# Kernel tuning notes

Hardware: AMD Instinct MI355X
Metric: run time of the kernel (lower is better)

## Reference

```python
import jax, jax.numpy as jnp
import numpy as np
from jax import lax

B, T, H = 4096, 2048, 32


def setup_inputs() -> dict:
    key = jax.random.key(0)
    ks = jax.random.split(key, 10)
    s = 1.0 / np.sqrt(H)  # PyTorch LSTM/Linear init scale
    x = jax.random.normal(ks[0], (B, T, 1), dtype=jnp.float32)
    lengths = jax.random.randint(ks[1], (B,), 1, T + 1, dtype=jnp.int32)
    u = lambda k, shape, sc: jax.random.uniform(k, shape, jnp.float32, -sc, sc)
    return {
        "x": x,
        "lengths": lengths,
        # backward-direction LSTM weights (only h_n[-1] is used by the head)
        "w_ih": u(ks[2], (4 * H, 1), s),
        "w_hh": u(ks[3], (4 * H, H), s),
        "b_ih": u(ks[4], (4 * H,), s),
        "b_hh": u(ks[5], (4 * H,), s),
        "fc_w": u(ks[6], (64, H), 1.0 / np.sqrt(H)),
        "fc_b": u(ks[7], (64,), 1.0 / np.sqrt(H)),
        "fc2_w": u(ks[8], (1, 64), 1.0 / np.sqrt(64)),
        "fc2_b": u(ks[9], (1,), 1.0 / np.sqrt(64)),
    }


def _backward_lstm_final(x, lengths, w_ih, w_hh, b_ih, b_hh):
    """Final hidden state of the backward direction of a packed BiLSTM.

    The backward direction reads each sequence from t=len-1 down to t=0 with
    zero initial state. Equivalently: scan padded x in reverse time order and
    only update (h, c) where t < length (packed-sequence semantics).
    """
    Bv, Tv, _ = x.shape
    ts = jnp.arange(Tv - 1, -1, -1)                       # reversed time indices
    xs_t = jnp.transpose(x[:, ::-1, :], (1, 0, 2))        # [T, B, 1]
    mask_t = ts[:, None] < lengths[None, :]               # [T, B]

    def step(carry, inp):
        h, c = carry
        xt, m = inp                                        # [B,1], [B]
        gates = xt @ w_ih.T + b_ih + h @ w_hh.T + b_hh     # [B, 4H]
        i, f, g, o = jnp.split(gates, 4, axis=-1)
        i = jax.nn.sigmoid(i)
        f = jax.nn.sigmoid(f)
        g = jnp.tanh(g)
        o = jax.nn.sigmoid(o)
        c_new = f * c + i * g
        h_new = o * jnp.tanh(c_new)
        mm = m[:, None]
        return (jnp.where(mm, h_new, h), jnp.where(mm, c_new, c)), None

    h0 = jnp.zeros((Bv, H), dtype=x.dtype)
    c0 = jnp.zeros((Bv, H), dtype=x.dtype)
    (h_n, _), _ = lax.scan(step, (h0, c0), (xs_t, mask_t))
    return h_n                                             # [B, H]


def reference(x, lengths, w_ih, w_hh, b_ih, b_hh, fc_w, fc_b, fc2_w, fc2_b):
    h_n = _backward_lstm_final(x, lengths, w_ih, w_hh, b_ih, b_hh)
    out = jax.nn.elu(h_n @ fc_w.T + fc_b)                  # [B, 64]
    out = jax.nn.sigmoid(out @ fc2_w.T + fc2_b)            # [B, 1]
    return out
```

## Files before the change

### kernel.cpp

```cpp
#include <hip/hip_runtime.h>
#include <hip/hip_bf16.h>

constexpr int BB = 4096;
constexpr int TT = 2048;
constexpr int HH = 32;

typedef float v2f __attribute__((ext_vector_type(2)));
typedef float v4f __attribute__((ext_vector_type(4)));
typedef _Float16 v2h __attribute__((ext_vector_type(2)));
typedef _Float16 v8h __attribute__((ext_vector_type(8)));

__device__ __forceinline__ float fexp2(float x) { return __builtin_amdgcn_exp2f(x); }
__device__ __forceinline__ float frcp(float x)  { return __builtin_amdgcn_rcpf(x); }
__device__ __forceinline__ float fsigmoid(float x) {
    return frcp(1.0f + fexp2(x * -1.4426950408889634f));
}
__device__ __forceinline__ float felu(float x) {
    return x > 0.0f ? x : (fexp2(x * 1.4426950408889634f) - 1.0f);
}

__global__ void sort_by_len_kernel(const int* __restrict__ lengths, int* __restrict__ perm) {
    __shared__ int hist[TT];
    __shared__ int csum[256];
    const int tid = threadIdx.x;
    for (int i = tid; i < TT; i += 256) hist[i] = 0;
    __syncthreads();
    for (int i = tid; i < BB; i += 256) atomicAdd(&hist[TT - lengths[i]], 1);
    __syncthreads();
    const int base = tid * 8;
    int loc[8];
    int s = 0;
#pragma unroll
    for (int j = 0; j < 8; ++j) { loc[j] = hist[base + j]; s += loc[j]; }
    csum[tid] = s;
    __syncthreads();
    for (int off = 1; off < 256; off <<= 1) {
        int v = (tid >= off) ? csum[tid - off] : 0;
        __syncthreads();
        csum[tid] += v;
        __syncthreads();
    }
    int run = csum[tid] - s;
#pragma unroll
    for (int j = 0; j < 8; ++j) { int t = loc[j]; hist[base + j] = run; run += t; }
    __syncthreads();
    for (int i = tid; i < BB; i += 256) {
        int pos = atomicAdd(&hist[TT - lengths[i]], 1);
        perm[pos] = i;
    }
}

__global__ __attribute__((amdgpu_flat_work_group_size(64, 64), amdgpu_waves_per_eu(1, 4)))
void lstm_kernel(const float* __restrict__ x, const int* __restrict__ lengths,
                 const float* __restrict__ w_ih, const float* __restrict__ w_hh,
                 const float* __restrict__ b_ih, const float* __restrict__ b_hh,
                 const float* __restrict__ fc_w, const float* __restrict__ fc_b,
                 const float* __restrict__ fc2_w, const float* __restrict__ fc2_b,
                 float* __restrict__ out, const int* __restrict__ perm) {
    __shared__ __align__(16) _Float16 hs[64];
    __shared__ float xbuf[64];

    const int lane = threadIdx.x;
    const int b = perm ? perm[blockIdx.x] : blockIdx.x;
    const int L = lengths[b];

    const int r0 = lane;
    const int r1 = lane + 64;

    const bool  lower  = lane < 32;
    const float NL2E   = -1.4426950408889634f;
    const float scale0 = NL2E;
    const float scale1 = lower ? 2.0f * NL2E : NL2E;
    const float amul   = lower ? 2.0f : 1.0f;
    const float badd   = lower ? -1.0f : 0.0f;

    v2h w0[16], w1[16];
    {
        const v2f* p0 = reinterpret_cast<const v2f*>(w_hh + r0 * 32);
        const v2f* p1 = reinterpret_cast<const v2f*>(w_hh + r1 * 32);
#pragma unroll
        for (int q = 0; q < 16; ++q) {
            v2f a = p0[q]; v2f bq = p1[q];
            w0[q] = (v2h){(_Float16)(a.x * scale0), (_Float16)(a.y * scale0)};
            w1[q] = (v2h){(_Float16)(bq.x * scale1), (_Float16)(bq.y * scale1)};
        }
    }
    float wi0 = w_ih[r0] * scale0;
    float wi1 = w_ih[r1] * scale1;
    float bi0 = (b_ih[r0] + b_hh[r0]) * scale0;
    float bi1 = (b_ih[r1] + b_hh[r1]) * scale1;

#pragma unroll
    for (int q = 0; q < 16; ++q) {
        asm volatile("" : "+v"(w0[q]), "+v"(w1[q]));
    }

    v8h hr[4];
#pragma unroll
    for (int q = 0; q < 4; ++q) hr[q] = (v8h)(_Float16)0.0f;
    float c = 0.0f;
    const float* xb = x + (size_t)b * TT;

    int t = L - 1;
    while (t >= 0) {
        const int tb = t & ~63;
        xbuf[lane] = xb[tb + lane];
        for (; t >= tb; --t) {
            const float xt = xbuf[t - tb];
            float a0  = fmaf(wi0, xt, bi0);
            float a1  = fmaf(wi1, xt, bi1);
            float a0b = 0.0f, a1b = 0.0f;
#pragma unroll
            for (int q = 0; q < 4; ++q) {
                const v8h hh = hr[q];
                const v2h p01 = __builtin_shufflevector(hh, hh, 0, 1);
                const v2h p23 = __builtin_shufflevector(hh, hh, 2, 3);
                const v2h p45 = __builtin_shufflevector(hh, hh, 4, 5);
                const v2h p67 = __builtin_shufflevector(hh, hh, 6, 7);
                a0  = __builtin_amdgcn_fdot2(w0[4*q+0], p01, a0,  false);
                a0b = __builtin_amdgcn_fdot2(w0[4*q+1], p23, a0b, false);
                a0  = __builtin_amdgcn_fdot2(w0[4*q+2], p45, a0,  false);
                a0b = __builtin_amdgcn_fdot2(w0[4*q+3], p67, a0b, false);
                a1  = __builtin_amdgcn_fdot2(w1[4*q+0], p01, a1,  false);
                a1b = __builtin_amdgcn_fdot2(w1[4*q+1], p23, a1b, false);
                a1  = __builtin_amdgcn_fdot2(w1[4*q+2], p45, a1,  false);
                a1b = __builtin_amdgcn_fdot2(w1[4*q+3], p67, a1b, false);
            }
            const float g0 = a0 + a0b;
            const float g1 = a1 + a1b;
            const float s0 = frcp(1.0f + fexp2(g0));
            const float s1 = frcp(1.0f + fexp2(g1));
            const float v1 = fmaf(amul, s1, badd);
            const float ig = s0 * v1;
            const float igx = __shfl_xor(ig, 32);
            c = fmaf(s0, c, igx);
            const float tc = 1.0f - 2.0f * frcp(1.0f + fexp2(c * 2.8853900817779268f));
            const float hn = v1 * tc;
            hs[lane] = (_Float16)hn;
            const v8h* hp = reinterpret_cast<const v8h*>(hs + 32);
#pragma unroll
            for (int q = 0; q < 4; ++q) hr[q] = hp[q];
        }
    }

    float hf[32];
#pragma unroll
    for (int q = 0; q < 4; ++q) {
        const v8h hh = hr[q];
#pragma unroll
        for (int j = 0; j < 8; ++j) hf[8 * q + j] = (float)hh[j];
    }
    float a = fc_b[lane];
    {
        const v4f* fp = reinterpret_cast<const v4f*>(fc_w + lane * 32);
#pragma unroll
        for (int q = 0; q < 8; ++q) {
            const v4f f = fp[q];
            a = fmaf(f.x, hf[4 * q + 0], a);
            a = fmaf(f.y, hf[4 * q + 1], a);
            a = fmaf(f.z, hf[4 * q + 2], a);
            a = fmaf(f.w, hf[4 * q + 3], a);
        }
    }
    float partial = felu(a) * fc2_w[lane];
#pragma unroll
    for (int m = 32; m >= 1; m >>= 1) partial += __shfl_xor(partial, m, 64);
    if (lane == 0) out[b] = fsigmoid(partial + fc2_b[0]);
}

extern "C" void kernel_launch(void* const* d_in, const int* in_sizes, int n_in,
                              void* d_out, int out_size, void* d_ws, size_t ws_size,
                              hipStream_t stream) {
    const float* x       = (const float*)d_in[0];
    const int*   lengths = (const int*)d_in[1];
    const float* w_ih    = (const float*)d_in[2];
    const float* w_hh    = (const float*)d_in[3];
    const float* b_ih    = (const float*)d_in[4];
    const float* b_hh    = (const float*)d_in[5];
    const float* fc_w    = (const float*)d_in[6];
    const float* fc_b    = (const float*)d_in[7];
    const float* fc2_w   = (const float*)d_in[8];
    const float* fc2_b   = (const float*)d_in[9];
    float* out = (float*)d_out;

    int* perm = nullptr;
    if (ws_size >= (size_t)BB * sizeof(int)) {
        perm = (int*)d_ws;
        hipLaunchKernelGGL(sort_by_len_kernel, dim3(1), dim3(256), 0, stream, lengths, perm);
    }
    hipLaunchKernelGGL(lstm_kernel, dim3(BB), dim3(64), 0, stream,
                       x, lengths, w_ih, w_hh, b_ih, b_hh,
                       fc_w, fc_b, fc2_w, fc2_b, out, perm);
}
```

Before: 645.7 us.

## Pack two sorted sequences per wave with one hidden unit per lane

Each 64-lane block now handles two length-adjacent sequences, one per half-wave, and each lane computes all four gates for one hidden unit. This removes the cross-half shuffle in the cell update and halves the number of blocks. The gate sigmoids and tanh are merged so two products share one reciprocal. In exchange each lane does twice the dot-product work per step and the shorter sequence runs masked steps up to the longer length. It also holds four weight arrays in registers, which raises register pressure.

```diff
diff --git a/kernel.cpp b/kernel.cpp
--- a/kernel.cpp
+++ b/kernel.cpp
@@ -1,5 +1,4 @@
 #include <hip/hip_runtime.h>
-#include <hip/hip_bf16.h>
 
 constexpr int BB = 4096;
 constexpr int TT = 2048;
@@ -50,94 +49,126 @@
     }
 }
 
-__global__ __attribute__((amdgpu_flat_work_group_size(64, 64), amdgpu_waves_per_eu(1, 4)))
+__global__ __attribute__((amdgpu_flat_work_group_size(64, 64)))
 void lstm_kernel(const float* __restrict__ x, const int* __restrict__ lengths,
                  const float* __restrict__ w_ih, const float* __restrict__ w_hh,
                  const float* __restrict__ b_ih, const float* __restrict__ b_hh,
                  const float* __restrict__ fc_w, const float* __restrict__ fc_b,
                  const float* __restrict__ fc2_w, const float* __restrict__ fc2_b,
                  float* __restrict__ out, const int* __restrict__ perm) {
-    __shared__ __align__(16) _Float16 hs[64];
-    __shared__ float xbuf[64];
+    __shared__ __align__(16) _Float16 hlds[64];
+    __shared__ float xbuf[128];
 
     const int lane = threadIdx.x;
-    const int b = perm ? perm[blockIdx.x] : blockIdx.x;
-    const int L = lengths[b];
-
-    const int r0 = lane;
-    const int r1 = lane + 64;
-
-    const bool  lower  = lane < 32;
-    const float NL2E   = -1.4426950408889634f;
-    const float scale0 = NL2E;
-    const float scale1 = lower ? 2.0f * NL2E : NL2E;
-    const float amul   = lower ? 2.0f : 1.0f;
-    const float badd   = lower ? -1.0f : 0.0f;
-
-    v2h w0[16], w1[16];
+    const int u = lane & 31;
+    const int e = lane >> 5;
+
+    const int k0 = 2 * blockIdx.x;
+    const int bA = perm ? perm[k0]     : k0;
+    const int bB = perm ? perm[k0 + 1] : k0 + 1;
+    const int LA = lengths[bA];
+    const int LB = lengths[bB];
+    const int Lme = e ? LB : LA;
+    const int bme = e ? bB : bA;
+    const int maxL = LA > LB ? LA : LB;
+
+    const float NL2E  = -1.4426950408889634f;
+    const float N2L2E = -2.8853900817779268f;
+
+    v2h wI[16], wF[16], wG[16], wO[16];
     {
-        const v2f* p0 = reinterpret_cast<const v2f*>(w_hh + r0 * 32);
-        const v2f* p1 = reinterpret_cast<const v2f*>(w_hh + r1 * 32);
+        const v2f* pI = reinterpret_cast<const v2f*>(w_hh + (u     ) * 32);
+        const v2f* pF = reinterpret_cast<const v2f*>(w_hh + (u + 32) * 32);
+        const v2f* pG = reinterpret_cast<const v2f*>(w_hh + (u + 64) * 32);
+        const v2f* pO = reinterpret_cast<const v2f*>(w_hh + (u + 96) * 32);
 #pragma unroll
         for (int q = 0; q < 16; ++q) {
-            v2f a = p0[q]; v2f bq = p1[q];
-            w0[q] = (v2h){(_Float16)(a.x * scale0), (_Float16)(a.y * scale0)};
-            w1[q] = (v2h){(_Float16)(bq.x * scale1), (_Float16)(bq.y * scale1)};
+            v2f ai = pI[q], af = pF[q], ag = pG[q], ao = pO[q];
+            wI[q] = (v2h){(_Float16)(ai.x * NL2E),  (_Float16)(ai.y * NL2E)};
+            wF[q] = (v2h){(_Float16)(af.x * NL2E),  (_Float16)(af.y * NL2E)};
+            wG[q] = (v2h){(_Float16)(ag.x * N2L2E), (_Float16)(ag.y * N2L2E)};
+            wO[q] = (v2h){(_Float16)(ao.x * NL2E),  (_Float16)(ao.y * NL2E)};
         }
     }
-    float wi0 = w_ih[r0] * scale0;
-    float wi1 = w_ih[r1] * scale1;
-    float bi0 = (b_ih[r0] + b_hh[r0]) * scale0;
-    float bi1 = (b_ih[r1] + b_hh[r1]) * scale1;
+    const float wiI = w_ih[u     ] * NL2E;
+    const float wiF = w_ih[u + 32] * NL2E;
+    const float wiG = w_ih[u + 64] * N2L2E;
+    const float wiO = w_ih[u + 96] * NL2E;
+    const float biI = (b_ih[u     ] + b_hh[u     ]) * NL2E;
+    const float biF = (b_ih[u + 32] + b_hh[u + 32]) * NL2E;
+    const float biG = (b_ih[u + 64] + b_hh[u + 64]) * N2L2E;
+    const float biO = (b_ih[u + 96] + b_hh[u + 96]) * NL2E;
 
 #pragma unroll
     for (int q = 0; q < 16; ++q) {
-        asm volatile("" : "+v"(w0[q]), "+v"(w1[q]));
+        asm volatile("" : "+v"(wI[q]), "+v"(wF[q]), "+v"(wG[q]), "+v"(wO[q]));
     }
 
     v8h hr[4];
 #pragma unroll
     for (int q = 0; q < 4; ++q) hr[q] = (v8h)(_Float16)0.0f;
     float c = 0.0f;
-    const float* xb = x + (size_t)b * TT;
-
-    int t = L - 1;
-    while (t >= 0) {
-        const int tb = t & ~63;
-        xbuf[lane] = xb[tb + lane];
-        for (; t >= tb; --t) {
-            const float xt = xbuf[t - tb];
-            float a0  = fmaf(wi0, xt, bi0);
-            float a1  = fmaf(wi1, xt, bi1);
-            float a0b = 0.0f, a1b = 0.0f;
+
+    const float* xA = x + (size_t)bA * TT;
+    const float* xB = x + (size_t)bB * TT;
+    const float* xme = xbuf + e * 64;
+    _Float16* hme = hlds + e * 32;
+
+    int s = maxL - 1;
+    while (s >= 0) {
+        const int tb = s & ~63;
+        xbuf[lane]      = xA[tb + lane];
+        xbuf[64 + lane] = xB[tb + lane];
+        for (; s >= tb; --s) {
+            const float xt = xme[s - tb];
+            float aI0 = fmaf(wiI, xt, biI), aI1 = 0.0f;
+            float aF0 = fmaf(wiF, xt, biF), aF1 = 0.0f;
+            float aG0 = fmaf(wiG, xt, biG), aG1 = 0.0f;
+            float aO0 = fmaf(wiO, xt, biO), aO1 = 0.0f;
 #pragma unroll
             for (int q = 0; q < 4; ++q) {
                 const v8h hh = hr[q];
-                const v2h p01 = __builtin_shufflevector(hh, hh, 0, 1);
-                const v2h p23 = __builtin_shufflevector(hh, hh, 2, 3);
-                const v2h p45 = __builtin_shufflevector(hh, hh, 4, 5);
-                const v2h p67 = __builtin_shufflevector(hh, hh, 6, 7);
-                a0  = __builtin_amdgcn_fdot2(w0[4*q+0], p01, a0,  false);
-                a0b = __builtin_amdgcn_fdot2(w0[4*q+1], p23, a0b, false);
-                a0  = __builtin_amdgcn_fdot2(w0[4*q+2], p45, a0,  false);
-                a0b = __builtin_amdgcn_fdot2(w0[4*q+3], p67, a0b, false);
-                a1  = __builtin_amdgcn_fdot2(w1[4*q+0], p01, a1,  false);
-                a1b = __builtin_amdgcn_fdot2(w1[4*q+1], p23, a1b, false);
-                a1  = __builtin_amdgcn_fdot2(w1[4*q+2], p45, a1,  false);
-                a1b = __builtin_amdgcn_fdot2(w1[4*q+3], p67, a1b, false);
+                const v2h p0 = __builtin_shufflevector(hh, hh, 0, 1);
+                const v2h p1 = __builtin_shufflevector(hh, hh, 2, 3);
+                const v2h p2 = __builtin_shufflevector(hh, hh, 4, 5);
+                const v2h p3 = __builtin_shufflevector(hh, hh, 6, 7);
+                aI0 = __builtin_amdgcn_fdot2(wI[4*q+0], p0, aI0, false);
+                aI1 = __builtin_amdgcn_fdot2(wI[4*q+1], p1, aI1, false);
+                aI0 = __builtin_amdgcn_fdot2(wI[4*q+2], p2, aI0, false);
+                aI1 = __builtin_amdgcn_fdot2(wI[4*q+3], p3, aI1, false);
+                aF0 = __builtin_amdgcn_fdot2(wF[4*q+0], p0, aF0, false);
+                aF1 = __builtin_amdgcn_fdot2(wF[4*q+1], p1, aF1, false);
+                aF0 = __builtin_amdgcn_fdot2(wF[4*q+2], p2, aF0, false);
+                aF1 = __builtin_amdgcn_fdot2(wF[4*q+3], p3, aF1, false);
+                aG0 = __builtin_amdgcn_fdot2(wG[4*q+0], p0, aG0, false);
+                aG1 = __builtin_amdgcn_fdot2(wG[4*q+1], p1, aG1, false);
+                aG0 = __builtin_amdgcn_fdot2(wG[4*q+2], p2, aG0, false);
+                aG1 = __builtin_amdgcn_fdot2(wG[4*q+3], p3, aG1, false);
+                aO0 = __builtin_amdgcn_fdot2(wO[4*q+0], p0, aO0, false);
+                aO1 = __builtin_amdgcn_fdot2(wO[4*q+1], p1, aO1, false);
+                aO0 = __builtin_amdgcn_fdot2(wO[4*q+2], p2, aO0, false);
+                aO1 = __builtin_amdgcn_fdot2(wO[4*q+3], p3, aO1, false);
             }
-            const float g0 = a0 + a0b;
-            const float g1 = a1 + a1b;
-            const float s0 = frcp(1.0f + fexp2(g0));
-            const float s1 = frcp(1.0f + fexp2(g1));
-            const float v1 = fmaf(amul, s1, badd);
-            const float ig = s0 * v1;
-            const float igx = __shfl_xor(ig, 32);
-            c = fmaf(s0, c, igx);
-            const float tc = 1.0f - 2.0f * frcp(1.0f + fexp2(c * 2.8853900817779268f));
-            const float hn = v1 * tc;
-            hs[lane] = (_Float16)hn;
-            const v8h* hp = reinterpret_cast<const v8h*>(hs + 32);
+            const float Ei = fexp2(aI0 + aI1);
+            const float Ef = fexp2(aF0 + aF1);
+            const float Eg = fexp2(aG0 + aG1);
+            const float Eo = fexp2(aO0 + aO1);
+            const float Ai = 1.0f + Ei, Ag = 1.0f + Eg;
+            const float Af = 1.0f + Ef, Ao = 1.0f + Eo;
+            const float R1 = frcp(Ai * Ag);
+            const float R2 = frcp(Af * Ao);
+            const float ig = (1.0f - Eg) * R1;
+            const float sf = R2 * Ao;
+            const float so = R2 * Af;
+            const float cn = fmaf(sf, c, ig);
+            const bool act = (s < Lme);
+            c = act ? cn : c;
+            const float carg = fminf(c * N2L2E, 126.0f);
+            const float Ec = fexp2(carg);
+            const float R3 = frcp(1.0f + Ec);
+            const float hn = so * ((1.0f - Ec) * R3);
+            hme[u] = (_Float16)(act ? hn : 0.0f);
+            const v8h* hp = reinterpret_cast<const v8h*>(hme);
 #pragma unroll
             for (int q = 0; q < 4; ++q) hr[q] = hp[q];
         }
@@ -150,22 +181,24 @@
 #pragma unroll
         for (int j = 0; j < 8; ++j) hf[8 * q + j] = (float)hh[j];
     }
-    float a = fc_b[lane];
+    float a0 = fc_b[u], a1 = fc_b[u + 32];
     {
-        const v4f* fp = reinterpret_cast<const v4f*>(fc_w + lane * 32);
+        const v4f* f0 = reinterpret_cast<const v4f*>(fc_w + u * 32);
+        const v4f* f1 = reinterpret_cast<const v4f*>(fc_w + (u + 32) * 32);
 #pragma unroll
         for (int q = 0; q < 8; ++q) {
-            const v4f f = fp[q];
-            a = fmaf(f.x, hf[4 * q + 0], a);
-            a = fmaf(f.y, hf[4 * q + 1], a);
-            a = fmaf(f.z, hf[4 * q + 2], a);
-            a = fmaf(f.w, hf[4 * q + 3], a);
+            const v4f fa = f0[q];
+            const v4f fb = f1[q];
+            a0 = fmaf(fa.x, hf[4*q+0], a0); a0 = fmaf(fa.y, hf[4*q+1], a0);
+            a0 = fmaf(fa.z, hf[4*q+2], a0); a0 = fmaf(fa.w, hf[4*q+3], a0);
+            a1 = fmaf(fb.x, hf[4*q+0], a1); a1 = fmaf(fb.y, hf[4*q+1], a1);
+            a1 = fmaf(fb.z, hf[4*q+2], a1); a1 = fmaf(fb.w, hf[4*q+3], a1);
         }
     }
-    float partial = felu(a) * fc2_w[lane];
-#pragma unroll
-    for (int m = 32; m >= 1; m >>= 1) partial += __shfl_xor(partial, m, 64);
-    if (lane == 0) out[b] = fsigmoid(partial + fc2_b[0]);
+    float partial = felu(a0) * fc2_w[u] + felu(a1) * fc2_w[u + 32];
+#pragma unroll
+    for (int m = 16; m >= 1; m >>= 1) partial += __shfl_xor(partial, m, 64);
+    if (u == 0) out[bme] = fsigmoid(partial + fc2_b[0]);
 }
 
 extern "C" void kernel_launch(void* const* d_in, const int* in_sizes, int n_in,
@@ -188,7 +221,7 @@
         perm = (int*)d_ws;
         hipLaunchKernelGGL(sort_by_len_kernel, dim3(1), dim3(256), 0, stream, lengths, perm);
     }
-    hipLaunchKernelGGL(lstm_kernel, dim3(BB), dim3(64), 0, stream,
+    hipLaunchKernelGGL(lstm_kernel, dim3(BB / 2), dim3(64), 0, stream,
                        x, lengths, w_ih, w_hh, b_ih, b_hh,
                        fc_w, fc_b, fc2_w, fc2_b, out, perm);
 }
```

Measured after the change: 721.0 us. 1.12x slower.

## Batch 16 sequences per block and compute LSTM recurrence with MFMA

Applied to the files above, without the earlier changes.

Replaces the one-sequence-per-wave fdot2 recurrence with blocks of 256 threads that process 16 length-sorted sequences together. The h·W_hh product runs on 16x16x32 f16 MFMA instructions, with gates laid out so each lane owns all four gates of two hidden units, and exp-based activations share reciprocals. Hidden state is double-buffered in LDS with one block barrier per step, and the loop runs to the group's maximum length with per-sequence masking. The intent is to swap per-lane dot products for matrix-core throughput, at the cost of a barrier every step, only 256 blocks, and wasted steps when lengths within a group differ.

```diff
diff --git a/kernel.cpp b/kernel.cpp
--- a/kernel.cpp
+++ b/kernel.cpp
@@ -1,12 +1,13 @@
 #include <hip/hip_runtime.h>
-#include <hip/hip_bf16.h>
 
 constexpr int BB = 4096;
 constexpr int TT = 2048;
 constexpr int HH = 32;
-
-typedef float v2f __attribute__((ext_vector_type(2)));
+constexpr int GE = 16;
+
 typedef float v4f __attribute__((ext_vector_type(4)));
+typedef float f32x4 __attribute__((ext_vector_type(4)));
+typedef _Float16 f16x8 __attribute__((ext_vector_type(8)));
 typedef _Float16 v2h __attribute__((ext_vector_type(2)));
 typedef _Float16 v8h __attribute__((ext_vector_type(8)));
 
@@ -50,122 +51,153 @@
     }
 }
 
-__global__ __attribute__((amdgpu_flat_work_group_size(64, 64), amdgpu_waves_per_eu(1, 4)))
+__global__ __attribute__((amdgpu_flat_work_group_size(256, 256)))
 void lstm_kernel(const float* __restrict__ x, const int* __restrict__ lengths,
                  const float* __restrict__ w_ih, const float* __restrict__ w_hh,
                  const float* __restrict__ b_ih, const float* __restrict__ b_hh,
                  const float* __restrict__ fc_w, const float* __restrict__ fc_b,
                  const float* __restrict__ fc2_w, const float* __restrict__ fc2_b,
                  float* __restrict__ out, const int* __restrict__ perm) {
-    __shared__ __align__(16) _Float16 hs[64];
-    __shared__ float xbuf[64];
-
-    const int lane = threadIdx.x;
-    const int b = perm ? perm[blockIdx.x] : blockIdx.x;
-    const int L = lengths[b];
-
-    const int r0 = lane;
-    const int r1 = lane + 64;
-
-    const bool  lower  = lane < 32;
-    const float NL2E   = -1.4426950408889634f;
-    const float scale0 = NL2E;
-    const float scale1 = lower ? 2.0f * NL2E : NL2E;
-    const float amul   = lower ? 2.0f : 1.0f;
-    const float badd   = lower ? -1.0f : 0.0f;
-
-    v2h w0[16], w1[16];
-    {
-        const v2f* p0 = reinterpret_cast<const v2f*>(w_hh + r0 * 32);
-        const v2f* p1 = reinterpret_cast<const v2f*>(w_hh + r1 * 32);
-#pragma unroll
-        for (int q = 0; q < 16; ++q) {
-            v2f a = p0[q]; v2f bq = p1[q];
-            w0[q] = (v2h){(_Float16)(a.x * scale0), (_Float16)(a.y * scale0)};
-            w1[q] = (v2h){(_Float16)(bq.x * scale1), (_Float16)(bq.y * scale1)};
-        }
-    }
-    float wi0 = w_ih[r0] * scale0;
-    float wi1 = w_ih[r1] * scale1;
-    float bi0 = (b_ih[r0] + b_hh[r0]) * scale0;
-    float bi1 = (b_ih[r1] + b_hh[r1]) * scale1;
-
-#pragma unroll
-    for (int q = 0; q < 16; ++q) {
-        asm volatile("" : "+v"(w0[q]), "+v"(w1[q]));
-    }
-
-    v8h hr[4];
-#pragma unroll
-    for (int q = 0; q < 4; ++q) hr[q] = (v8h)(_Float16)0.0f;
-    float c = 0.0f;
-    const float* xb = x + (size_t)b * TT;
-
-    int t = L - 1;
-    while (t >= 0) {
-        const int tb = t & ~63;
-        xbuf[lane] = xb[tb + lane];
-        for (; t >= tb; --t) {
-            const float xt = xbuf[t - tb];
-            float a0  = fmaf(wi0, xt, bi0);
-            float a1  = fmaf(wi1, xt, bi1);
-            float a0b = 0.0f, a1b = 0.0f;
-#pragma unroll
-            for (int q = 0; q < 4; ++q) {
-                const v8h hh = hr[q];
-                const v2h p01 = __builtin_shufflevector(hh, hh, 0, 1);
-                const v2h p23 = __builtin_shufflevector(hh, hh, 2, 3);
-                const v2h p45 = __builtin_shufflevector(hh, hh, 4, 5);
-                const v2h p67 = __builtin_shufflevector(hh, hh, 6, 7);
-                a0  = __builtin_amdgcn_fdot2(w0[4*q+0], p01, a0,  false);
-                a0b = __builtin_amdgcn_fdot2(w0[4*q+1], p23, a0b, false);
-                a0  = __builtin_amdgcn_fdot2(w0[4*q+2], p45, a0,  false);
-                a0b = __builtin_amdgcn_fdot2(w0[4*q+3], p67, a0b, false);
-                a1  = __builtin_amdgcn_fdot2(w1[4*q+0], p01, a1,  false);
-                a1b = __builtin_amdgcn_fdot2(w1[4*q+1], p23, a1b, false);
-                a1  = __builtin_amdgcn_fdot2(w1[4*q+2], p45, a1,  false);
-                a1b = __builtin_amdgcn_fdot2(w1[4*q+3], p67, a1b, false);
-            }
-            const float g0 = a0 + a0b;
-            const float g1 = a1 + a1b;
-            const float s0 = frcp(1.0f + fexp2(g0));
-            const float s1 = frcp(1.0f + fexp2(g1));
-            const float v1 = fmaf(amul, s1, badd);
-            const float ig = s0 * v1;
-            const float igx = __shfl_xor(ig, 32);
-            c = fmaf(s0, c, igx);
-            const float tc = 1.0f - 2.0f * frcp(1.0f + fexp2(c * 2.8853900817779268f));
-            const float hn = v1 * tc;
-            hs[lane] = (_Float16)hn;
-            const v8h* hp = reinterpret_cast<const v8h*>(hs + 32);
-#pragma unroll
-            for (int q = 0; q < 4; ++q) hr[q] = hp[q];
-        }
-    }
-
-    float hf[32];
-#pragma unroll
-    for (int q = 0; q < 4; ++q) {
-        const v8h hh = hr[q];
-#pragma unroll
-        for (int j = 0; j < 8; ++j) hf[8 * q + j] = (float)hh[j];
-    }
-    float a = fc_b[lane];
-    {
+    __shared__ __align__(16) _Float16 hb[2][GE][40];
+    __shared__ __align__(16) float xls[GE][68];
+    __shared__ int barr[GE];
+    __shared__ int Llds[GE];
+    __shared__ int maxLs;
+
+    const int tid  = threadIdx.x;
+    const int wv   = tid >> 6;
+    const int lane = tid & 63;
+    const int lg   = lane >> 4;
+    const int e    = lane & 15;
+
+    const int g = blockIdx.x;
+    if (tid < GE) {
+        const int b = perm ? perm[GE * g + tid] : (GE * g + tid);
+        barr[tid] = b;
+        Llds[tid] = lengths[b];
+    }
+    for (int i = tid; i < 2 * GE * 40; i += 256) ((_Float16*)hb)[i] = (_Float16)0.0f;
+    __syncthreads();
+    if (tid == 0) {
+        int m = 0;
+        for (int i = 0; i < GE; ++i) m = max(m, Llds[i]);
+        maxLs = m;
+    }
+    __syncthreads();
+    const int maxL = maxLs;
+    const int Lme  = Llds[e];
+
+    const float NL2E = -1.4426950408889634f;
+
+    const int r = lane & 15;
+    const int sgate = r & 3;
+    const int qq = r >> 2;
+    const float asc = (sgate == 2) ? 2.0f * NL2E : NL2E;
+    f16x8 afr[2];
+#pragma unroll
+    for (int m = 0; m < 2; ++m) {
+        const int u = 8 * wv + 2 * qq + m;
+        const int wrow = sgate * 32 + u;
+        const v4f* wp = reinterpret_cast<const v4f*>(w_hh + wrow * 32 + 8 * lg);
+        const v4f wa = wp[0], wb = wp[1];
+        afr[m] = (f16x8){(_Float16)(wa.x * asc), (_Float16)(wa.y * asc),
+                         (_Float16)(wa.z * asc), (_Float16)(wa.w * asc),
+                         (_Float16)(wb.x * asc), (_Float16)(wb.y * asc),
+                         (_Float16)(wb.z * asc), (_Float16)(wb.w * asc)};
+    }
+    float wih_[2][4], bs_[2][4];
+#pragma unroll
+    for (int m = 0; m < 2; ++m) {
+        const int u = 8 * wv + 2 * lg + m;
+#pragma unroll
+        for (int i = 0; i < 4; ++i) {
+            const float scd = (i == 2) ? 2.0f * NL2E : NL2E;
+            wih_[m][i] = w_ih[i * 32 + u] * scd;
+            bs_[m][i]  = (b_ih[i * 32 + u] + b_hh[i * 32 + u]) * scd;
+        }
+    }
+
+    float c0 = 0.0f, c1 = 0.0f;
+    int p = 0;
+    const int hoff = 8 * wv + 2 * lg;
+
+    for (int s = maxL - 1; s >= 0; --s) {
+        if (s == maxL - 1 || (s & 63) == 63) {
+            const int tb = s & ~63;
+            const int es = tid >> 4, j4 = (tid & 15) * 4;
+            const float* xp = x + (size_t)barr[es] * TT + tb + j4;
+            *reinterpret_cast<v4f*>(&xls[es][j4]) = *reinterpret_cast<const v4f*>(xp);
+            __syncthreads();
+        }
+        const f16x8 bf = *reinterpret_cast<const f16x8*>(&hb[p][e][lg * 8]);
+        const float xe = xls[e][s & 63];
+        f32x4 C0, C1;
+#pragma unroll
+        for (int i = 0; i < 4; ++i) {
+            C0[i] = fmaf(wih_[0][i], xe, bs_[0][i]);
+            C1[i] = fmaf(wih_[1][i], xe, bs_[1][i]);
+        }
+        const f32x4 D0 = __builtin_amdgcn_mfma_f32_16x16x32_f16(afr[0], bf, C0, 0, 0, 0);
+        const f32x4 D1 = __builtin_amdgcn_mfma_f32_16x16x32_f16(afr[1], bf, C1, 0, 0, 0);
+        const bool act = (s < Lme);
+
+        float h0, h1;
+        {
+            const float Ei = fexp2(D0[0]), Ef = fexp2(D0[1]);
+            const float Eg = fexp2(D0[2]), Eo = fexp2(D0[3]);
+            const float R1 = frcp((1.0f + Ei) * (1.0f + Eg));
+            const float ig = (1.0f - Eg) * R1;
+            const float R2 = frcp((1.0f + Ef) * (1.0f + Eo));
+            const float sf = (1.0f + Eo) * R2;
+            const float so = (1.0f + Ef) * R2;
+            const float cn = fmaf(sf, c0, ig);
+            c0 = act ? cn : c0;
+            const float tc = 1.0f - 2.0f * frcp(1.0f + fexp2(c0 * 2.8853900817779268f));
+            h0 = act ? (so * tc) : 0.0f;
+        }
+        {
+            const float Ei = fexp2(D1[0]), Ef = fexp2(D1[1]);
+            const float Eg = fexp2(D1[2]), Eo = fexp2(D1[3]);
+            const float R1 = frcp((1.0f + Ei) * (1.0f + Eg));
+            const float ig = (1.0f - Eg) * R1;
+            const float R2 = frcp((1.0f + Ef) * (1.0f + Eo));
+            const float sf = (1.0f + Eo) * R2;
+            const float so = (1.0f + Ef) * R2;
+            const float cn = fmaf(sf, c1, ig);
+            c1 = act ? cn : c1;
+            const float tc = 1.0f - 2.0f * frcp(1.0f + fexp2(c1 * 2.8853900817779268f));
+            h1 = act ? (so * tc) : 0.0f;
+        }
+        const v2h pk = {(_Float16)h0, (_Float16)h1};
+        *reinterpret_cast<v2h*>(&hb[p ^ 1][e][hoff]) = pk;
+        __syncthreads();
+        p ^= 1;
+    }
+
+    for (int e2 = 4 * wv; e2 < 4 * wv + 4; ++e2) {
+        float hf[32];
+        const v8h* hp8 = reinterpret_cast<const v8h*>(&hb[p][e2][0]);
+#pragma unroll
+        for (int q4 = 0; q4 < 4; ++q4) {
+            const v8h hh = hp8[q4];
+#pragma unroll
+            for (int j = 0; j < 8; ++j) hf[8 * q4 + j] = (float)hh[j];
+        }
+        float a = fc_b[lane];
         const v4f* fp = reinterpret_cast<const v4f*>(fc_w + lane * 32);
 #pragma unroll
-        for (int q = 0; q < 8; ++q) {
-            const v4f f = fp[q];
-            a = fmaf(f.x, hf[4 * q + 0], a);
-            a = fmaf(f.y, hf[4 * q + 1], a);
-            a = fmaf(f.z, hf[4 * q + 2], a);
-            a = fmaf(f.w, hf[4 * q + 3], a);
-        }
-    }
-    float partial = felu(a) * fc2_w[lane];
-#pragma unroll
-    for (int m = 32; m >= 1; m >>= 1) partial += __shfl_xor(partial, m, 64);
-    if (lane == 0) out[b] = fsigmoid(partial + fc2_b[0]);
+        for (int q4 = 0; q4 < 8; ++q4) {
+            const v4f f = fp[q4];
+            a = fmaf(f.x, hf[4 * q4 + 0], a);
+            a = fmaf(f.y, hf[4 * q4 + 1], a);
+            a = fmaf(f.z, hf[4 * q4 + 2], a);
+            a = fmaf(f.w, hf[4 * q4 + 3], a);
+        }
+        float partial = felu(a) * fc2_w[lane];
+#pragma unroll
+        for (int m = 32; m >= 1; m >>= 1) partial += __shfl_xor(partial, m, 64);
+        if (lane == 0) out[barr[e2]] = fsigmoid(partial + fc2_b[0]);
+    }
 }
 
 extern "C" void kernel_launch(void* const* d_in, const int* in_sizes, int n_in,
@@ -188,7 +220,7 @@
         perm = (int*)d_ws;
         hipLaunchKernelGGL(sort_by_len_kernel, dim3(1), dim3(256), 0, stream, lengths, perm);
     }
-    hipLaunchKernelGGL(lstm_kernel, dim3(BB), dim3(64), 0, stream,
+    hipLaunchKernelGGL(lstm_kernel, dim3(BB / GE), dim3(256), 0, stream,
                        x, lengths, w_ih, w_hh, b_ih, b_hh,
                        fc_w, fc_b, fc2_w, fc2_b, out, perm);
 }
```

Result: slower. 676.6 us (+4.8%).
